# Optimization experiments

Hardware: AMD Instinct MI355X
Metric: run time of the kernel (lower is better)

Reference implementation:

```python
import jax, jax.numpy as jnp
import numpy as np

B, NF, N, D, S, H = 16, 16, 1024, 128, 8, 128
EPS = 1e-8
SCALE = D ** -0.5


def _ln(x, g, b):
    m = x.mean(-1, keepdims=True)
    v = ((x - m) ** 2).mean(-1, keepdims=True)
    return (x - m) / jnp.sqrt(v + 1e-5) * g + b


def setup_inputs() -> dict:
    key = jax.random.key(0)
    ks = jax.random.split(key, 16)
    w = lambda k, *s: jax.random.normal(k, s, jnp.float32) * 0.02
    return {
        'inputs': jax.random.normal(ks[0], (B, NF, N, D), jnp.float32),
        'slots_init': jax.random.normal(ks[1], (1, S, D), jnp.float32),
        'Wq': w(ks[2], D, D), 'bq': jnp.zeros((D,), jnp.float32),
        'Wk': w(ks[3], D, D), 'bk': jnp.zeros((D,), jnp.float32),
        'Wv': w(ks[4], D, D), 'bv': jnp.zeros((D,), jnp.float32),
        'W1': w(ks[5], H, D), 'b1': jnp.zeros((H,), jnp.float32),
        'W2': w(ks[6], D, H), 'b2': jnp.zeros((D,), jnp.float32),
        'Wih': w(ks[7], 3 * D, D), 'Whh': w(ks[8], 3 * D, D),
        'bih': jnp.zeros((3 * D,), jnp.float32), 'bhh': jnp.zeros((3 * D,), jnp.float32),
        'g_in': jnp.ones((D,), jnp.float32), 'be_in': jnp.zeros((D,), jnp.float32),
        'g_sl': jnp.ones((D,), jnp.float32), 'be_sl': jnp.zeros((D,), jnp.float32),
        'g_ff': jnp.ones((D,), jnp.float32), 'be_ff': jnp.zeros((D,), jnp.float32),
    }


def reference(inputs, slots_init, Wq, bq, Wk, bk, Wv, bv, W1, b1, W2, b2,
              Wih, Whh, bih, bhh, g_in, be_in, g_sl, be_sl, g_ff, be_ff):
    def gru(x, h):  # PyTorch GRUCell, x/h: [BS, D]
        gi = x @ Wih.T + bih
        gh = h @ Whh.T + bhh
        r = jax.nn.sigmoid(gi[:, :D] + gh[:, :D])
        z = jax.nn.sigmoid(gi[:, D:2 * D] + gh[:, D:2 * D])
        n = jnp.tanh(gi[:, 2 * D:] + r * gh[:, 2 * D:])
        return (1.0 - z) * n + z * h

    def get_attention(slots, x):  # slots [B,S,D], x [B,N,D]
        slots_prev = slots
        xn = _ln(x, g_in, be_in)
        k = xn @ Wk.T + bk
        v = xn @ Wv.T + bv
        q = _ln(slots, g_sl, be_sl) @ Wq.T + bq
        dots = jnp.einsum('bid,bjd->bij', q, k) * SCALE  # [B,S,N]
        attn_ori = jax.nn.softmax(dots, axis=1) + EPS    # softmax over slots
        attn = attn_ori / attn_ori.sum(axis=-1, keepdims=True)
        updates = jnp.einsum('bjd,bij->bid', v, attn)    # [B,S,D]
        slots = gru(updates.reshape(-1, D), slots_prev.reshape(-1, D)).reshape(slots.shape[0], -1, D)
        ff = jax.nn.relu(_ln(slots, g_ff, be_ff) @ W1.T + b1) @ W2.T + b2
        return slots + ff, attn_ori

    slots = jnp.broadcast_to(slots_init, (inputs.shape[0], S, D))
    slots, _ = get_attention(slots, inputs[:, 0])  # warm-up on frame 0

    def body(carry, x_f):
        s, a = get_attention(carry, x_f)
        return s, (s, a)

    _, (slots_seq, attn_seq) = jax.lax.scan(body, slots, jnp.moveaxis(inputs, 1, 0))
    slots_out = jnp.moveaxis(slots_seq, 0, 1)  # [B,NF,S,D]
    attns = jnp.moveaxis(attn_seq, 0, 1)       # [B,NF,S,N]
    return slots_out, attns
```

## Files before the change

kernel.cpp:

```cpp
#include <hip/hip_runtime.h>

#define B_ 16
#define NF_ 16
#define N_ 1024
#define D_ 128
#define S_ 8
#define SCALE_ 0.08838834764831845f
#define LDX 129

__device__ __forceinline__ float dot128f(const float* __restrict__ wrow, const float* x, float acc) {
  const float4* w = (const float4*)wrow;
#pragma unroll
  for (int i = 0; i < 32; ++i) {
    float4 v = w[i];
    const float* xx = x + i * 4;
    acc += v.x * xx[0] + v.y * xx[1] + v.z * xx[2] + v.w * xx[3];
  }
  return acc;
}

__device__ __forceinline__ void stats128(float v, int t, float* red, float& m, float& inv, float eps) {
  __syncthreads();
  float s = (t < 128) ? v : 0.f;
  float s2 = (t < 128) ? v * v : 0.f;
#pragma unroll
  for (int off = 32; off; off >>= 1) { s += __shfl_down(s, off); s2 += __shfl_down(s2, off); }
  if (t == 0)  { red[0] = s; red[2] = s2; }
  if (t == 64) { red[1] = s; red[3] = s2; }
  __syncthreads();
  m = (red[0] + red[1]) * (1.f / 128.f);
  float var = (red[2] + red[3]) * (1.f / 128.f) - m * m;
  inv = rsqrtf(var + eps);
}

__device__ __forceinline__ void project_q(const float* q_sh, const float* __restrict__ Wk,
    const float* __restrict__ bk, float* red, int t, int bs,
    float* __restrict__ qW, float* __restrict__ qb) {
  if (t < 128) {
    float a = 0.f;
#pragma unroll 16
    for (int d = 0; d < 128; ++d) a += q_sh[d] * Wk[d * 128 + t];
    qW[bs * 128 + t] = a;
    float p = q_sh[t] * bk[t];
#pragma unroll
    for (int off = 32; off; off >>= 1) p += __shfl_down(p, off);
    if (t == 0)  red[0] = p;
    if (t == 64) red[1] = p;
  }
  __syncthreads();
  if (t == 0) qb[bs] = red[0] + red[1];
}

__global__ __launch_bounds__(128) void init_kernel(
    const float* __restrict__ slots_init,
    const float* __restrict__ g_sl, const float* __restrict__ be_sl,
    const float* __restrict__ Wq, const float* __restrict__ bq,
    const float* __restrict__ Wk, const float* __restrict__ bk,
    float* __restrict__ slots, float* __restrict__ qW, float* __restrict__ qb) {
  int t = threadIdx.x;
  int b = blockIdx.x >> 3, s = blockIdx.x & 7;
  __shared__ float buf[128], q_sh[128];
  __shared__ float red[4];
  float v = slots_init[s * 128 + t];
  slots[(b * 8 + s) * 128 + t] = v;
  float m, inv;
  stats128(v, t, red, m, inv, 1e-5f);
  buf[t] = (v - m) * inv * g_sl[t] + be_sl[t];
  __syncthreads();
  q_sh[t] = dot128f(Wq + t * 128, buf, bq[t]);
  __syncthreads();
  project_q(q_sh, Wk, bk, red, t, b * 8 + s, qW, qb);
}

__global__ __launch_bounds__(256) void attn_kernel(
    const float* __restrict__ x,
    const float* __restrict__ g_in, const float* __restrict__ be_in,
    const float* __restrict__ qW, const float* __restrict__ qb,
    float* __restrict__ P_part, float* __restrict__ S_part,
    float* __restrict__ out_attn, int f, int wo) {
  __shared__ float Xt[64 * LDX];
  __shared__ float qWs[8 * 128];
  __shared__ float at[8 * 64];
  __shared__ float qbs[8];
  __shared__ float rowsum[64], rowsum2[64];
  int t = threadIdx.x;
  int b = blockIdx.x >> 4, jt = blockIdx.x & 15;
  long xbase = (((long)b * NF_ + f) * N_ + jt * 64) * D_;

#pragma unroll
  for (int i = 0; i < 8; ++i) {
    int chunk = t + i * 256;
    int r = chunk >> 5, c = (chunk & 31) * 4;
    float4 raw = *(const float4*)(x + xbase + r * D_ + c);
    float* dst = Xt + r * LDX + c;
    dst[0] = raw.x; dst[1] = raw.y; dst[2] = raw.z; dst[3] = raw.w;
  }
#pragma unroll
  for (int i = 0; i < 4; ++i) {
    int idx = t + i * 256;
    qWs[idx] = qW[b * (S_ * D_) + idx];
  }
  if (t < 8) qbs[t] = qb[b * 8 + t];
  __syncthreads();

  int r = t >> 2, p4 = t & 3;
  {
    const float* row = Xt + r * LDX + p4 * 32;
    float s1 = 0.f, s2 = 0.f;
#pragma unroll
    for (int i = 0; i < 32; ++i) { float v = row[i]; s1 += v; s2 += v * v; }
    s1 += __shfl_down(s1, 1); s2 += __shfl_down(s2, 1);
    s1 += __shfl_down(s1, 2); s2 += __shfl_down(s2, 2);
    if (p4 == 0) { rowsum[r] = s1; rowsum2[r] = s2; }
  }
  __syncthreads();
  {
    float m = rowsum[r] * (1.f / 128.f);
    float var = rowsum2[r] * (1.f / 128.f) - m * m;
    float inv = rsqrtf(var + 1e-5f);
    float* row = Xt + r * LDX + p4 * 32;
    const float* gg = g_in + p4 * 32;
    const float* bb = be_in + p4 * 32;
#pragma unroll
    for (int i = 0; i < 32; ++i)
      row[i] = (row[i] - m) * inv * gg[i] + bb[i];
  }
  __syncthreads();

  {
    int j = t & 63, sh = t >> 6;
    const float* q0 = qWs + (2 * sh) * 128;
    const float* q1 = qWs + (2 * sh + 1) * 128;
    const float* xr = Xt + j * LDX;
    float d0 = 0.f, d1 = 0.f;
#pragma unroll
    for (int k = 0; k < 128; ++k) {
      float xv = xr[k];
      d0 += xv * q0[k];
      d1 += xv * q1[k];
    }
    at[(2 * sh) * 64 + j]     = (d0 + qbs[2 * sh])     * SCALE_;
    at[(2 * sh + 1) * 64 + j] = (d1 + qbs[2 * sh + 1]) * SCALE_;
  }
  __syncthreads();

  if (t < 64) {
    float vals[8];
    float mx = -1e30f;
#pragma unroll
    for (int s = 0; s < 8; ++s) { vals[s] = at[s * 64 + t]; mx = fmaxf(mx, vals[s]); }
    float sum = 0.f;
#pragma unroll
    for (int s = 0; s < 8; ++s) { vals[s] = __expf(vals[s] - mx); sum += vals[s]; }
    float rr = 1.f / sum;
#pragma unroll
    for (int s = 0; s < 8; ++s) {
      vals[s] = vals[s] * rr + 1e-8f;
      at[s * 64 + t] = vals[s];
    }
    if (wo) {
#pragma unroll
      for (int s = 0; s < 8; ++s)
        out_attn[(((long)b * NF_ + f) * S_ + s) * N_ + jt * 64 + t] = vals[s];
    }
#pragma unroll
    for (int s = 0; s < 8; ++s) {
      float v = vals[s];
#pragma unroll
      for (int off = 32; off; off >>= 1) v += __shfl_down(v, off);
      if (t == 0) S_part[(b * 16 + jt) * 8 + s] = v;
    }
  }
  __syncthreads();

  {
    int k = t & 127, h = t >> 7;
    float u0 = 0.f, u1 = 0.f, u2 = 0.f, u3 = 0.f;
    const float* a0 = at + (h * 4 + 0) * 64;
    const float* a1 = at + (h * 4 + 1) * 64;
    const float* a2 = at + (h * 4 + 2) * 64;
    const float* a3 = at + (h * 4 + 3) * 64;
#pragma unroll 8
    for (int j = 0; j < 64; ++j) {
      float xv = Xt[j * LDX + k];
      u0 += xv * a0[j]; u1 += xv * a1[j]; u2 += xv * a2[j]; u3 += xv * a3[j];
    }
    float* pp = P_part + (long)(b * 16 + jt) * 8 * 128;
    pp[(h * 4 + 0) * 128 + k] = u0;
    pp[(h * 4 + 1) * 128 + k] = u1;
    pp[(h * 4 + 2) * 128 + k] = u2;
    pp[(h * 4 + 3) * 128 + k] = u3;
  }
}

__global__ __launch_bounds__(384) void update_kernel(
    const float* __restrict__ P_part, const float* __restrict__ S_part,
    const float* __restrict__ Wih, const float* __restrict__ Whh,
    const float* __restrict__ bih, const float* __restrict__ bhh,
    const float* __restrict__ W1, const float* __restrict__ b1,
    const float* __restrict__ W2, const float* __restrict__ b2,
    const float* __restrict__ g_ff, const float* __restrict__ be_ff,
    const float* __restrict__ g_sl, const float* __restrict__ be_sl,
    const float* __restrict__ Wq, const float* __restrict__ bq,
    const float* __restrict__ Wk, const float* __restrict__ bk,
    const float* __restrict__ Wv, const float* __restrict__ bv,
    float* __restrict__ slots, float* __restrict__ qW, float* __restrict__ qb,
    float* __restrict__ out_slots, int f, int wo) {
  int t = threadIdx.x;
  int b = blockIdx.x >> 3, s = blockIdx.x & 7;
  __shared__ float Pk[128], hprev[128], upd[128], hn[128], buf[128], hid[128], q_sh[128];
  __shared__ float giS[384], ghS[384];
  __shared__ float red[4];

  if (t < 128) {
    float pa = 0.f;
#pragma unroll
    for (int jt = 0; jt < 16; ++jt) pa += P_part[((b * 16 + jt) * 8 + s) * 128 + t];
    float ss = 0.f;
#pragma unroll
    for (int jt = 0; jt < 16; ++jt) ss += S_part[(b * 16 + jt) * 8 + s];
    Pk[t] = pa / ss;
    hprev[t] = slots[(b * 8 + s) * 128 + t];
  }
  __syncthreads();
  if (t < 128) upd[t] = dot128f(Wv + t * 128, Pk, bv[t]);
  __syncthreads();
  giS[t] = dot128f(Wih + t * 128, upd, bih[t]);
  ghS[t] = dot128f(Whh + t * 128, hprev, bhh[t]);
  __syncthreads();
  if (t < 128) {
    float r = 1.f / (1.f + expf(-(giS[t] + ghS[t])));
    float z = 1.f / (1.f + expf(-(giS[128 + t] + ghS[128 + t])));
    float n = tanhf(giS[256 + t] + r * ghS[256 + t]);
    hn[t] = (1.f - z) * n + z * hprev[t];
  }
  __syncthreads();
  float m, inv;
  float hv = (t < 128) ? hn[t] : 0.f;
  stats128(hv, t, red, m, inv, 1e-5f);
  if (t < 128) buf[t] = (hv - m) * inv * g_ff[t] + be_ff[t];
  __syncthreads();
  if (t < 128) hid[t] = fmaxf(dot128f(W1 + t * 128, buf, b1[t]), 0.f);
  __syncthreads();
  if (t < 128) {
    float ffv = dot128f(W2 + t * 128, hid, b2[t]);
    float sn = hn[t] + ffv;
    slots[(b * 8 + s) * 128 + t] = sn;
    if (wo) out_slots[(((long)b * NF_ + f) * S_ + s) * 128 + t] = sn;
    buf[t] = sn;
  }
  __syncthreads();
  float sv = (t < 128) ? buf[t] : 0.f;
  stats128(sv, t, red, m, inv, 1e-5f);
  if (t < 128) hid[t] = (sv - m) * inv * g_sl[t] + be_sl[t];
  __syncthreads();
  if (t < 128) q_sh[t] = dot128f(Wq + t * 128, hid, bq[t]);
  __syncthreads();
  project_q(q_sh, Wk, bk, red, t, b * 8 + s, qW, qb);
}

extern "C" void kernel_launch(void* const* d_in, const int* in_sizes, int n_in,
                              void* d_out, int out_size, void* d_ws, size_t ws_size,
                              hipStream_t stream) {
  const float* inputs     = (const float*)d_in[0];
  const float* slots_init = (const float*)d_in[1];
  const float* Wq  = (const float*)d_in[2];
  const float* bq  = (const float*)d_in[3];
  const float* Wk  = (const float*)d_in[4];
  const float* bk  = (const float*)d_in[5];
  const float* Wv  = (const float*)d_in[6];
  const float* bv  = (const float*)d_in[7];
  const float* W1  = (const float*)d_in[8];
  const float* b1  = (const float*)d_in[9];
  const float* W2  = (const float*)d_in[10];
  const float* b2  = (const float*)d_in[11];
  const float* Wih = (const float*)d_in[12];
  const float* Whh = (const float*)d_in[13];
  const float* bih = (const float*)d_in[14];
  const float* bhh = (const float*)d_in[15];
  const float* g_in  = (const float*)d_in[16];
  const float* be_in = (const float*)d_in[17];
  const float* g_sl  = (const float*)d_in[18];
  const float* be_sl = (const float*)d_in[19];
  const float* g_ff  = (const float*)d_in[20];
  const float* be_ff = (const float*)d_in[21];

  float* out_slots = (float*)d_out;
  float* out_attn  = out_slots + (size_t)B_ * NF_ * S_ * D_;

  char* ws = (char*)d_ws;
  float* slots  = (float*)(ws);
  float* qW     = (float*)(ws + 65536);
  float* qb     = (float*)(ws + 131072);
  float* P_part = (float*)(ws + 131584);
  float* S_part = (float*)(ws + 131584 + 1048576);

  init_kernel<<<128, 128, 0, stream>>>(slots_init, g_sl, be_sl, Wq, bq, Wk, bk,
                                       slots, qW, qb);

  for (int it = 0; it < 17; ++it) {
    int f = (it == 0) ? 0 : it - 1;
    int wo = (it > 0) ? 1 : 0;
    attn_kernel<<<256, 256, 0, stream>>>(inputs, g_in, be_in, qW, qb,
                                         P_part, S_part, out_attn, f, wo);
    update_kernel<<<128, 384, 0, stream>>>(P_part, S_part, Wih, Whh, bih, bhh,
        W1, b1, W2, b2, g_ff, be_ff, g_sl, be_sl, Wq, bq, Wk, bk, Wv, bv,
        slots, qW, qb, out_slots, f, wo);
  }
}
```

Before: 819.3 us.

## Fuse all iterations into one persistent kernel with grid-wide barriers

Replaces the 35 separate kernel launches (init plus 17 attention and update pairs) with a single persistent kernel of 256 blocks that synchronises through an atomic-counter grid barrier. Each update block now handles all 8 slots of a batch at once, which shares weight rows across slots, and the next frame's input tile is prefetched into registers while the update phase runs. The intent is to remove launch overhead and the global round-trips of slot state. In exchange it depends on all 256 blocks being co-resident, since a spinning barrier otherwise deadlocks. Only 16 blocks do the serial update while the other 240 wait.

```diff
diff --git a/kernel.cpp b/kernel.cpp
--- a/kernel.cpp
+++ b/kernel.cpp
@@ -6,257 +6,354 @@
 #define D_ 128
 #define S_ 8
 #define SCALE_ 0.08838834764831845f
-#define LDX 129
-
-__device__ __forceinline__ float dot128f(const float* __restrict__ wrow, const float* x, float acc) {
-  const float4* w = (const float4*)wrow;
-#pragma unroll
+#define NB 256
+#define NT 512
+
+struct SmemA {
+  float Xt[64 * 129];
+  float qWs[1024];
+  float at[512];
+  float rowsum[64], rowsum2[64];
+  float qbs[8];
+};
+struct SmemB {
+  float Pk[1024], upd[1024], hn[1024], buf[1024], hid[1024], qsh[1024];
+  float gi[3072], gh[3072];
+  float mst[8], ist[8], ssm[8];
+};
+union Smem { SmemA a; SmemB b; };
+
+__device__ __forceinline__ void grid_sync(unsigned* cnt, unsigned epoch) {
+  __syncthreads();
+  if (threadIdx.x == 0) {
+    __threadfence();
+    __hip_atomic_fetch_add(cnt, 1u, __ATOMIC_RELAXED, __HIP_MEMORY_SCOPE_AGENT);
+    unsigned target = NB * epoch;
+    while (__hip_atomic_load(cnt, __ATOMIC_RELAXED, __HIP_MEMORY_SCOPE_AGENT) < target)
+      __builtin_amdgcn_s_sleep(1);
+    __threadfence();
+  }
+  __syncthreads();
+}
+
+__device__ __forceinline__ void stats8(const float* arr, float* mst, float* ist, float eps) {
+  __syncthreads();
+  int w = threadIdx.x >> 6, lane = threadIdx.x & 63;
+  float v0 = arr[w * 128 + lane], v1 = arr[w * 128 + 64 + lane];
+  float s1 = v0 + v1, s2 = v0 * v0 + v1 * v1;
+#pragma unroll
+  for (int off = 32; off; off >>= 1) { s1 += __shfl_down(s1, off); s2 += __shfl_down(s2, off); }
+  if (lane == 0) {
+    float m = s1 * (1.f / 128.f);
+    float var = s2 * (1.f / 128.f) - m * m;
+    mst[w] = m; ist[w] = rsqrtf(var + eps);
+  }
+  __syncthreads();
+}
+
+__device__ __forceinline__ void dorow8(const float* __restrict__ wrow, float bias,
+                                       const float* v, float* out, int o) {
+  float acc[8];
+#pragma unroll
+  for (int s = 0; s < 8; ++s) acc[s] = bias;
+  const float4* wr = (const float4*)wrow;
+#pragma unroll 8
   for (int i = 0; i < 32; ++i) {
-    float4 v = w[i];
-    const float* xx = x + i * 4;
-    acc += v.x * xx[0] + v.y * xx[1] + v.z * xx[2] + v.w * xx[3];
-  }
-  return acc;
-}
-
-__device__ __forceinline__ void stats128(float v, int t, float* red, float& m, float& inv, float eps) {
-  __syncthreads();
-  float s = (t < 128) ? v : 0.f;
-  float s2 = (t < 128) ? v * v : 0.f;
-#pragma unroll
-  for (int off = 32; off; off >>= 1) { s += __shfl_down(s, off); s2 += __shfl_down(s2, off); }
-  if (t == 0)  { red[0] = s; red[2] = s2; }
-  if (t == 64) { red[1] = s; red[3] = s2; }
-  __syncthreads();
-  m = (red[0] + red[1]) * (1.f / 128.f);
-  float var = (red[2] + red[3]) * (1.f / 128.f) - m * m;
-  inv = rsqrtf(var + eps);
-}
-
-__device__ __forceinline__ void project_q(const float* q_sh, const float* __restrict__ Wk,
-    const float* __restrict__ bk, float* red, int t, int bs,
-    float* __restrict__ qW, float* __restrict__ qb) {
+    float4 wv = wr[i];
+#pragma unroll
+    for (int s = 0; s < 8; ++s) {
+      float4 xv = *(const float4*)(v + s * 128 + i * 4);
+      acc[s] += wv.x * xv.x + wv.y * xv.y + wv.z * xv.z + wv.w * xv.w;
+    }
+  }
+#pragma unroll
+  for (int s = 0; s < 8; ++s) out[s * 384 + o] = acc[s];
+}
+
+__device__ __forceinline__ float sigm(float x) { return 1.f / (1.f + __expf(-x)); }
+__device__ __forceinline__ float tanh_f(float x) { return 1.f - 2.f / (1.f + __expf(2.f * x)); }
+
+__device__ void slots_to_q(SmemB& B, const float* slot_sh,
+    const float* g_sl, const float* be_sl, const float* Wq, const float* bq,
+    const float* Wk, const float* bk, float* qW_g, float* qb_g, int b) {
+  int t = threadIdx.x, k = t & 127, sp = t >> 7;
+  stats8(slot_sh, B.mst, B.ist, 1e-5f);
   if (t < 128) {
-    float a = 0.f;
+    float g = g_sl[t], be = be_sl[t];
+#pragma unroll
+    for (int s = 0; s < 8; ++s)
+      B.buf[s * 128 + t] = (slot_sh[s * 128 + t] - B.mst[s]) * B.ist[s] * g + be;
+  }
+  __syncthreads();
+  {
+    float a0 = bq[k], a1 = bq[k];
+    const float4* wr = (const float4*)(Wq + k * 128);
+#pragma unroll 8
+    for (int i = 0; i < 32; ++i) {
+      float4 wv = wr[i];
+      float4 x0 = *(const float4*)(B.buf + sp * 128 + i * 4);
+      float4 x1 = *(const float4*)(B.buf + (sp + 4) * 128 + i * 4);
+      a0 += wv.x * x0.x + wv.y * x0.y + wv.z * x0.z + wv.w * x0.w;
+      a1 += wv.x * x1.x + wv.y * x1.y + wv.z * x1.z + wv.w * x1.w;
+    }
+    B.qsh[sp * 128 + k] = a0; B.qsh[(sp + 4) * 128 + k] = a1;
+  }
+  __syncthreads();
+  {
+    float a0 = 0.f, a1 = 0.f;
 #pragma unroll 16
-    for (int d = 0; d < 128; ++d) a += q_sh[d] * Wk[d * 128 + t];
-    qW[bs * 128 + t] = a;
-    float p = q_sh[t] * bk[t];
-#pragma unroll
-    for (int off = 32; off; off >>= 1) p += __shfl_down(p, off);
-    if (t == 0)  red[0] = p;
-    if (t == 64) red[1] = p;
-  }
-  __syncthreads();
-  if (t == 0) qb[bs] = red[0] + red[1];
-}
-
-__global__ __launch_bounds__(128) void init_kernel(
-    const float* __restrict__ slots_init,
-    const float* __restrict__ g_sl, const float* __restrict__ be_sl,
-    const float* __restrict__ Wq, const float* __restrict__ bq,
-    const float* __restrict__ Wk, const float* __restrict__ bk,
-    float* __restrict__ slots, float* __restrict__ qW, float* __restrict__ qb) {
-  int t = threadIdx.x;
-  int b = blockIdx.x >> 3, s = blockIdx.x & 7;
-  __shared__ float buf[128], q_sh[128];
-  __shared__ float red[4];
-  float v = slots_init[s * 128 + t];
-  slots[(b * 8 + s) * 128 + t] = v;
-  float m, inv;
-  stats128(v, t, red, m, inv, 1e-5f);
-  buf[t] = (v - m) * inv * g_sl[t] + be_sl[t];
-  __syncthreads();
-  q_sh[t] = dot128f(Wq + t * 128, buf, bq[t]);
-  __syncthreads();
-  project_q(q_sh, Wk, bk, red, t, b * 8 + s, qW, qb);
-}
-
-__global__ __launch_bounds__(256) void attn_kernel(
-    const float* __restrict__ x,
-    const float* __restrict__ g_in, const float* __restrict__ be_in,
-    const float* __restrict__ qW, const float* __restrict__ qb,
-    float* __restrict__ P_part, float* __restrict__ S_part,
-    float* __restrict__ out_attn, int f, int wo) {
-  __shared__ float Xt[64 * LDX];
-  __shared__ float qWs[8 * 128];
-  __shared__ float at[8 * 64];
-  __shared__ float qbs[8];
-  __shared__ float rowsum[64], rowsum2[64];
-  int t = threadIdx.x;
-  int b = blockIdx.x >> 4, jt = blockIdx.x & 15;
-  long xbase = (((long)b * NF_ + f) * N_ + jt * 64) * D_;
-
-#pragma unroll
-  for (int i = 0; i < 8; ++i) {
-    int chunk = t + i * 256;
-    int r = chunk >> 5, c = (chunk & 31) * 4;
-    float4 raw = *(const float4*)(x + xbase + r * D_ + c);
-    float* dst = Xt + r * LDX + c;
-    dst[0] = raw.x; dst[1] = raw.y; dst[2] = raw.z; dst[3] = raw.w;
-  }
-#pragma unroll
-  for (int i = 0; i < 4; ++i) {
-    int idx = t + i * 256;
-    qWs[idx] = qW[b * (S_ * D_) + idx];
-  }
-  if (t < 8) qbs[t] = qb[b * 8 + t];
-  __syncthreads();
-
-  int r = t >> 2, p4 = t & 3;
+    for (int d = 0; d < 128; ++d) {
+      float wv = Wk[d * 128 + k];
+      a0 += B.qsh[sp * 128 + d] * wv;
+      a1 += B.qsh[(sp + 4) * 128 + d] * wv;
+    }
+    qW_g[(b * 8 + sp) * 128 + k] = a0;
+    qW_g[(b * 8 + sp + 4) * 128 + k] = a1;
+  }
+  if (t < 128) {
+    float bkt = bk[t];
+#pragma unroll
+    for (int s = 0; s < 8; ++s) B.hid[s * 128 + t] = B.qsh[s * 128 + t] * bkt;
+  }
+  __syncthreads();
   {
-    const float* row = Xt + r * LDX + p4 * 32;
-    float s1 = 0.f, s2 = 0.f;
-#pragma unroll
-    for (int i = 0; i < 32; ++i) { float v = row[i]; s1 += v; s2 += v * v; }
-    s1 += __shfl_down(s1, 1); s2 += __shfl_down(s2, 1);
-    s1 += __shfl_down(s1, 2); s2 += __shfl_down(s2, 2);
-    if (p4 == 0) { rowsum[r] = s1; rowsum2[r] = s2; }
-  }
-  __syncthreads();
-  {
-    float m = rowsum[r] * (1.f / 128.f);
-    float var = rowsum2[r] * (1.f / 128.f) - m * m;
-    float inv = rsqrtf(var + 1e-5f);
-    float* row = Xt + r * LDX + p4 * 32;
-    const float* gg = g_in + p4 * 32;
-    const float* bb = be_in + p4 * 32;
-#pragma unroll
-    for (int i = 0; i < 32; ++i)
-      row[i] = (row[i] - m) * inv * gg[i] + bb[i];
-  }
-  __syncthreads();
-
-  {
-    int j = t & 63, sh = t >> 6;
-    const float* q0 = qWs + (2 * sh) * 128;
-    const float* q1 = qWs + (2 * sh + 1) * 128;
-    const float* xr = Xt + j * LDX;
-    float d0 = 0.f, d1 = 0.f;
-#pragma unroll
-    for (int k = 0; k < 128; ++k) {
-      float xv = xr[k];
-      d0 += xv * q0[k];
-      d1 += xv * q1[k];
-    }
-    at[(2 * sh) * 64 + j]     = (d0 + qbs[2 * sh])     * SCALE_;
-    at[(2 * sh + 1) * 64 + j] = (d1 + qbs[2 * sh + 1]) * SCALE_;
-  }
-  __syncthreads();
-
-  if (t < 64) {
-    float vals[8];
-    float mx = -1e30f;
-#pragma unroll
-    for (int s = 0; s < 8; ++s) { vals[s] = at[s * 64 + t]; mx = fmaxf(mx, vals[s]); }
-    float sum = 0.f;
-#pragma unroll
-    for (int s = 0; s < 8; ++s) { vals[s] = __expf(vals[s] - mx); sum += vals[s]; }
-    float rr = 1.f / sum;
-#pragma unroll
-    for (int s = 0; s < 8; ++s) {
-      vals[s] = vals[s] * rr + 1e-8f;
-      at[s * 64 + t] = vals[s];
-    }
-    if (wo) {
-#pragma unroll
-      for (int s = 0; s < 8; ++s)
-        out_attn[(((long)b * NF_ + f) * S_ + s) * N_ + jt * 64 + t] = vals[s];
-    }
-#pragma unroll
-    for (int s = 0; s < 8; ++s) {
-      float v = vals[s];
-#pragma unroll
-      for (int off = 32; off; off >>= 1) v += __shfl_down(v, off);
-      if (t == 0) S_part[(b * 16 + jt) * 8 + s] = v;
-    }
-  }
-  __syncthreads();
-
-  {
-    int k = t & 127, h = t >> 7;
-    float u0 = 0.f, u1 = 0.f, u2 = 0.f, u3 = 0.f;
-    const float* a0 = at + (h * 4 + 0) * 64;
-    const float* a1 = at + (h * 4 + 1) * 64;
-    const float* a2 = at + (h * 4 + 2) * 64;
-    const float* a3 = at + (h * 4 + 3) * 64;
-#pragma unroll 8
-    for (int j = 0; j < 64; ++j) {
-      float xv = Xt[j * LDX + k];
-      u0 += xv * a0[j]; u1 += xv * a1[j]; u2 += xv * a2[j]; u3 += xv * a3[j];
-    }
-    float* pp = P_part + (long)(b * 16 + jt) * 8 * 128;
-    pp[(h * 4 + 0) * 128 + k] = u0;
-    pp[(h * 4 + 1) * 128 + k] = u1;
-    pp[(h * 4 + 2) * 128 + k] = u2;
-    pp[(h * 4 + 3) * 128 + k] = u3;
-  }
-}
-
-__global__ __launch_bounds__(384) void update_kernel(
-    const float* __restrict__ P_part, const float* __restrict__ S_part,
-    const float* __restrict__ Wih, const float* __restrict__ Whh,
-    const float* __restrict__ bih, const float* __restrict__ bhh,
-    const float* __restrict__ W1, const float* __restrict__ b1,
-    const float* __restrict__ W2, const float* __restrict__ b2,
-    const float* __restrict__ g_ff, const float* __restrict__ be_ff,
-    const float* __restrict__ g_sl, const float* __restrict__ be_sl,
+    int w = t >> 6, lane = t & 63;
+    float s1 = B.hid[w * 128 + lane] + B.hid[w * 128 + 64 + lane];
+#pragma unroll
+    for (int off = 32; off; off >>= 1) s1 += __shfl_down(s1, off);
+    if (lane == 0) qb_g[b * 8 + w] = s1;
+  }
+}
+
+__global__ __launch_bounds__(NT) void slot_persist(
+    const float* __restrict__ x, const float* __restrict__ slots_init,
     const float* __restrict__ Wq, const float* __restrict__ bq,
     const float* __restrict__ Wk, const float* __restrict__ bk,
     const float* __restrict__ Wv, const float* __restrict__ bv,
-    float* __restrict__ slots, float* __restrict__ qW, float* __restrict__ qb,
-    float* __restrict__ out_slots, int f, int wo) {
-  int t = threadIdx.x;
-  int b = blockIdx.x >> 3, s = blockIdx.x & 7;
-  __shared__ float Pk[128], hprev[128], upd[128], hn[128], buf[128], hid[128], q_sh[128];
-  __shared__ float giS[384], ghS[384];
-  __shared__ float red[4];
-
-  if (t < 128) {
-    float pa = 0.f;
-#pragma unroll
-    for (int jt = 0; jt < 16; ++jt) pa += P_part[((b * 16 + jt) * 8 + s) * 128 + t];
-    float ss = 0.f;
-#pragma unroll
-    for (int jt = 0; jt < 16; ++jt) ss += S_part[(b * 16 + jt) * 8 + s];
-    Pk[t] = pa / ss;
-    hprev[t] = slots[(b * 8 + s) * 128 + t];
-  }
-  __syncthreads();
-  if (t < 128) upd[t] = dot128f(Wv + t * 128, Pk, bv[t]);
-  __syncthreads();
-  giS[t] = dot128f(Wih + t * 128, upd, bih[t]);
-  ghS[t] = dot128f(Whh + t * 128, hprev, bhh[t]);
-  __syncthreads();
-  if (t < 128) {
-    float r = 1.f / (1.f + expf(-(giS[t] + ghS[t])));
-    float z = 1.f / (1.f + expf(-(giS[128 + t] + ghS[128 + t])));
-    float n = tanhf(giS[256 + t] + r * ghS[256 + t]);
-    hn[t] = (1.f - z) * n + z * hprev[t];
-  }
-  __syncthreads();
-  float m, inv;
-  float hv = (t < 128) ? hn[t] : 0.f;
-  stats128(hv, t, red, m, inv, 1e-5f);
-  if (t < 128) buf[t] = (hv - m) * inv * g_ff[t] + be_ff[t];
-  __syncthreads();
-  if (t < 128) hid[t] = fmaxf(dot128f(W1 + t * 128, buf, b1[t]), 0.f);
-  __syncthreads();
-  if (t < 128) {
-    float ffv = dot128f(W2 + t * 128, hid, b2[t]);
-    float sn = hn[t] + ffv;
-    slots[(b * 8 + s) * 128 + t] = sn;
-    if (wo) out_slots[(((long)b * NF_ + f) * S_ + s) * 128 + t] = sn;
-    buf[t] = sn;
-  }
-  __syncthreads();
-  float sv = (t < 128) ? buf[t] : 0.f;
-  stats128(sv, t, red, m, inv, 1e-5f);
-  if (t < 128) hid[t] = (sv - m) * inv * g_sl[t] + be_sl[t];
-  __syncthreads();
-  if (t < 128) q_sh[t] = dot128f(Wq + t * 128, hid, bq[t]);
-  __syncthreads();
-  project_q(q_sh, Wk, bk, red, t, b * 8 + s, qW, qb);
+    const float* __restrict__ W1, const float* __restrict__ b1,
+    const float* __restrict__ W2, const float* __restrict__ b2,
+    const float* __restrict__ Wih, const float* __restrict__ Whh,
+    const float* __restrict__ bih, const float* __restrict__ bhh,
+    const float* __restrict__ g_in, const float* __restrict__ be_in,
+    const float* __restrict__ g_sl, const float* __restrict__ be_sl,
+    const float* __restrict__ g_ff, const float* __restrict__ be_ff,
+    float* out_slots, float* out_attn,
+    unsigned* cnt, float* qW_g, float* qb_g, float* P_part, float* S_part) {
+  __shared__ __align__(16) Smem sm;
+  __shared__ __align__(16) float slot_sh[1024];
+  __shared__ float gs[128], bs_[128];
+  int t = threadIdx.x, bid = blockIdx.x;
+  int b_a = bid >> 4, jt = bid & 15;
+
+  if (t < 128) { gs[t] = g_in[t]; bs_[t] = be_in[t]; }
+  if (bid < 16) {
+    if (t < 128) {
+#pragma unroll
+      for (int s = 0; s < 8; ++s) slot_sh[s * 128 + t] = slots_init[s * 128 + t];
+    }
+    slots_to_q(sm.b, slot_sh, g_sl, be_sl, Wq, bq, Wk, bk, qW_g, qb_g, bid);
+  }
+  float4 pf[4];
+  {
+    const float* xsrc = x + (((long)b_a * NF_ + 0) * N_ + jt * 64) * D_;
+#pragma unroll
+    for (int i = 0; i < 4; ++i) {
+      int ch = t + i * 512;
+      pf[i] = *(const float4*)(xsrc + (ch >> 5) * 128 + (ch & 31) * 4);
+    }
+  }
+  grid_sync(cnt, 1);
+
+  for (int it = 0; it < 17; ++it) {
+    int f = (it == 0) ? 0 : it - 1;
+    int wo = it > 0;
+#pragma unroll
+    for (int i = 0; i < 4; ++i) {
+      int ch = t + i * 512;
+      float* dst = sm.a.Xt + (ch >> 5) * 129 + (ch & 31) * 4;
+      dst[0] = pf[i].x; dst[1] = pf[i].y; dst[2] = pf[i].z; dst[3] = pf[i].w;
+    }
+    sm.a.qWs[t] = qW_g[b_a * 1024 + t];
+    sm.a.qWs[512 + t] = qW_g[b_a * 1024 + 512 + t];
+    if (t < 8) sm.a.qbs[t] = qb_g[b_a * 8 + t];
+    __syncthreads();
+    int r8 = t >> 3, p8 = t & 7;
+    {
+      const float* row = sm.a.Xt + r8 * 129 + p8 * 16;
+      float s1 = 0.f, s2 = 0.f;
+#pragma unroll
+      for (int i = 0; i < 16; ++i) { float v = row[i]; s1 += v; s2 += v * v; }
+      s1 += __shfl_down(s1, 1); s2 += __shfl_down(s2, 1);
+      s1 += __shfl_down(s1, 2); s2 += __shfl_down(s2, 2);
+      s1 += __shfl_down(s1, 4); s2 += __shfl_down(s2, 4);
+      if (p8 == 0) { sm.a.rowsum[r8] = s1; sm.a.rowsum2[r8] = s2; }
+    }
+    __syncthreads();
+    {
+      float m = sm.a.rowsum[r8] * (1.f / 128.f);
+      float var = sm.a.rowsum2[r8] * (1.f / 128.f) - m * m;
+      float inv = rsqrtf(var + 1e-5f);
+      float* row = sm.a.Xt + r8 * 129 + p8 * 16;
+      const float* gg = gs + p8 * 16;
+      const float* bb = bs_ + p8 * 16;
+#pragma unroll
+      for (int i = 0; i < 16; ++i) row[i] = (row[i] - m) * inv * gg[i] + bb[i];
+    }
+    __syncthreads();
+    {
+      int s = t >> 6, j = t & 63;
+      const float* qq = sm.a.qWs + s * 128;
+      const float* xr = sm.a.Xt + j * 129;
+      float d = 0.f;
+#pragma unroll
+      for (int k = 0; k < 128; ++k) d += xr[k] * qq[k];
+      sm.a.at[s * 64 + j] = (d + sm.a.qbs[s]) * SCALE_;
+    }
+    __syncthreads();
+    if (t < 64) {
+      float vals[8], mx = -1e30f;
+#pragma unroll
+      for (int s = 0; s < 8; ++s) { vals[s] = sm.a.at[s * 64 + t]; mx = fmaxf(mx, vals[s]); }
+      float sum = 0.f;
+#pragma unroll
+      for (int s = 0; s < 8; ++s) { vals[s] = __expf(vals[s] - mx); sum += vals[s]; }
+      float rr = 1.f / sum;
+#pragma unroll
+      for (int s = 0; s < 8; ++s) { vals[s] = vals[s] * rr + 1e-8f; sm.a.at[s * 64 + t] = vals[s]; }
+      if (wo) {
+#pragma unroll
+        for (int s = 0; s < 8; ++s)
+          out_attn[(((long)b_a * NF_ + f) * S_ + s) * N_ + jt * 64 + t] = vals[s];
+      }
+    }
+    __syncthreads();
+    {
+      int w = t >> 6, lane = t & 63;
+      float v = sm.a.at[w * 64 + lane];
+#pragma unroll
+      for (int off = 32; off; off >>= 1) v += __shfl_down(v, off);
+      if (lane == 0) S_part[(b_a * 16 + jt) * 8 + w] = v;
+    }
+    {
+      int k2 = t & 127, h = t >> 7;
+      float u0 = 0.f, u1 = 0.f;
+      const float* a0 = sm.a.at + h * 64;
+      const float* a1 = sm.a.at + (h + 4) * 64;
+#pragma unroll 8
+      for (int j = 0; j < 64; ++j) {
+        float xv = sm.a.Xt[j * 129 + k2];
+        u0 += xv * a0[j]; u1 += xv * a1[j];
+      }
+      float* pp = P_part + (long)(b_a * 16 + jt) * 8 * 128;
+      pp[h * 128 + k2] = u0;
+      pp[(h + 4) * 128 + k2] = u1;
+    }
+    grid_sync(cnt, 2 + 2 * it);
+    if (it < 16) {
+      const float* xsrc = x + (((long)b_a * NF_ + it) * N_ + jt * 64) * D_;
+#pragma unroll
+      for (int i = 0; i < 4; ++i) {
+        int ch = t + i * 512;
+        pf[i] = *(const float4*)(xsrc + (ch >> 5) * 128 + (ch & 31) * 4);
+      }
+    }
+    if (bid < 16) {
+      int b = bid, k = t & 127, sp = t >> 7;
+      SmemB& B = sm.b;
+      float pa0 = 0.f, pa1 = 0.f;
+#pragma unroll
+      for (int j = 0; j < 16; ++j) {
+        const float* pp = P_part + (long)(b * 16 + j) * 8 * 128;
+        pa0 += pp[sp * 128 + k];
+        pa1 += pp[(sp + 4) * 128 + k];
+      }
+      if (t < 8) {
+        float ss = 0.f;
+#pragma unroll
+        for (int j = 0; j < 16; ++j) ss += S_part[(b * 16 + j) * 8 + t];
+        B.ssm[t] = ss;
+      }
+      __syncthreads();
+      B.Pk[sp * 128 + k] = pa0 / B.ssm[sp];
+      B.Pk[(sp + 4) * 128 + k] = pa1 / B.ssm[sp + 4];
+      __syncthreads();
+      {
+        float a0 = bv[k], a1 = bv[k];
+        const float4* wr = (const float4*)(Wv + k * 128);
+#pragma unroll 8
+        for (int i = 0; i < 32; ++i) {
+          float4 wv = wr[i];
+          float4 x0 = *(const float4*)(B.Pk + sp * 128 + i * 4);
+          float4 x1 = *(const float4*)(B.Pk + (sp + 4) * 128 + i * 4);
+          a0 += wv.x * x0.x + wv.y * x0.y + wv.z * x0.z + wv.w * x0.w;
+          a1 += wv.x * x1.x + wv.y * x1.y + wv.z * x1.z + wv.w * x1.w;
+        }
+        B.upd[sp * 128 + k] = a0; B.upd[(sp + 4) * 128 + k] = a1;
+      }
+      __syncthreads();
+      if (t < 384) dorow8(Wih + t * 128, bih[t], B.upd, B.gi, t);
+      {
+        int rh = (t >= 384) ? (t - 384) : (t < 256 ? 128 + t : -1);
+        if (rh >= 0) dorow8(Whh + rh * 128, bhh[rh], slot_sh, B.gh, rh);
+      }
+      __syncthreads();
+      if (t < 128) {
+#pragma unroll
+        for (int s = 0; s < 8; ++s) {
+          float r = sigm(B.gi[s * 384 + t] + B.gh[s * 384 + t]);
+          float z = sigm(B.gi[s * 384 + 128 + t] + B.gh[s * 384 + 128 + t]);
+          float n = tanh_f(B.gi[s * 384 + 256 + t] + r * B.gh[s * 384 + 256 + t]);
+          B.hn[s * 128 + t] = (1.f - z) * n + z * slot_sh[s * 128 + t];
+        }
+      }
+      stats8(B.hn, B.mst, B.ist, 1e-5f);
+      if (t < 128) {
+        float g = g_ff[t], be = be_ff[t];
+#pragma unroll
+        for (int s = 0; s < 8; ++s)
+          B.buf[s * 128 + t] = (B.hn[s * 128 + t] - B.mst[s]) * B.ist[s] * g + be;
+      }
+      __syncthreads();
+      {
+        float a0 = b1[k], a1 = b1[k];
+        const float4* wr = (const float4*)(W1 + k * 128);
+#pragma unroll 8
+        for (int i = 0; i < 32; ++i) {
+          float4 wv = wr[i];
+          float4 x0 = *(const float4*)(B.buf + sp * 128 + i * 4);
+          float4 x1 = *(const float4*)(B.buf + (sp + 4) * 128 + i * 4);
+          a0 += wv.x * x0.x + wv.y * x0.y + wv.z * x0.z + wv.w * x0.w;
+          a1 += wv.x * x1.x + wv.y * x1.y + wv.z * x1.z + wv.w * x1.w;
+        }
+        B.hid[sp * 128 + k] = fmaxf(a0, 0.f);
+        B.hid[(sp + 4) * 128 + k] = fmaxf(a1, 0.f);
+      }
+      __syncthreads();
+      {
+        float a0 = b2[k], a1 = b2[k];
+        const float4* wr = (const float4*)(W2 + k * 128);
+#pragma unroll 8
+        for (int i = 0; i < 32; ++i) {
+          float4 wv = wr[i];
+          float4 x0 = *(const float4*)(B.hid + sp * 128 + i * 4);
+          float4 x1 = *(const float4*)(B.hid + (sp + 4) * 128 + i * 4);
+          a0 += wv.x * x0.x + wv.y * x0.y + wv.z * x0.z + wv.w * x0.w;
+          a1 += wv.x * x1.x + wv.y * x1.y + wv.z * x1.z + wv.w * x1.w;
+        }
+        float sn0 = B.hn[sp * 128 + k] + a0;
+        float sn1 = B.hn[(sp + 4) * 128 + k] + a1;
+        slot_sh[sp * 128 + k] = sn0;
+        slot_sh[(sp + 4) * 128 + k] = sn1;
+        if (wo) {
+          out_slots[(((long)b * NF_ + f) * S_ + sp) * D_ + k] = sn0;
+          out_slots[(((long)b * NF_ + f) * S_ + sp + 4) * D_ + k] = sn1;
+        }
+      }
+      if (it < 16)
+        slots_to_q(B, slot_sh, g_sl, be_sl, Wq, bq, Wk, bk, qW_g, qb_g, b);
+    }
+    if (it < 16) grid_sync(cnt, 3 + 2 * it);
+  }
 }
 
 extern "C" void kernel_launch(void* const* d_in, const int* in_sizes, int n_in,
@@ -289,22 +386,15 @@
   float* out_attn  = out_slots + (size_t)B_ * NF_ * S_ * D_;
 
   char* ws = (char*)d_ws;
-  float* slots  = (float*)(ws);
-  float* qW     = (float*)(ws + 65536);
-  float* qb     = (float*)(ws + 131072);
-  float* P_part = (float*)(ws + 131584);
-  float* S_part = (float*)(ws + 131584 + 1048576);
-
-  init_kernel<<<128, 128, 0, stream>>>(slots_init, g_sl, be_sl, Wq, bq, Wk, bk,
-                                       slots, qW, qb);
-
-  for (int it = 0; it < 17; ++it) {
-    int f = (it == 0) ? 0 : it - 1;
-    int wo = (it > 0) ? 1 : 0;
-    attn_kernel<<<256, 256, 0, stream>>>(inputs, g_in, be_in, qW, qb,
-                                         P_part, S_part, out_attn, f, wo);
-    update_kernel<<<128, 384, 0, stream>>>(P_part, S_part, Wih, Whh, bih, bhh,
-        W1, b1, W2, b2, g_ff, be_ff, g_sl, be_sl, Wq, bq, Wk, bk, Wv, bv,
-        slots, qW, qb, out_slots, f, wo);
-  }
-}
+  unsigned* cnt  = (unsigned*)ws;
+  float* qW_g    = (float*)(ws + 1024);
+  float* qb_g    = (float*)(ws + 1024 + 65536);
+  float* P_part  = (float*)(ws + 67072);
+  float* S_part  = (float*)(ws + 67072 + 1048576);
+
+  hipMemsetAsync(d_ws, 0, 256, stream);
+
+  slot_persist<<<NB, NT, 0, stream>>>(inputs, slots_init, Wq, bq, Wk, bk, Wv, bv,
+      W1, b1, W2, b2, Wih, Whh, bih, bhh, g_in, be_in, g_sl, be_sl, g_ff, be_ff,
+      out_slots, out_attn, cnt, qW_g, qb_g, P_part, S_part);
+}
```

Measured after the change: 1.969 ms. 140% more time.
